# Optimization experiments

Measured on AMD Instinct MI355X. Metric: run time of the kernel, lower is better.

The kernel has to match this reference:

```python
import jax, jax.numpy as jnp
import numpy as np

B, T, C = 32, 128, 64
E, H = 8, 4            # feat_dim, num_heads
D = E // H             # head_dim = 2
HID = 32               # hidden_dim


def setup_inputs() -> dict:
    key = jax.random.key(0)
    ks = jax.random.split(key, 20)
    s = 0.1
    return {
        "x": jax.random.normal(ks[0], (B, T, C), jnp.float32),
        # input_proj: Linear(C, C)
        "W_in": jax.random.normal(ks[1], (C, C), jnp.float32) * s,
        "b_in": jax.random.normal(ks[2], (C,), jnp.float32) * s,
        # time_step_score: Linear(C, C//4) -> GELU -> Linear(C//4, 1) -> Sigmoid
        "W_ts1": jax.random.normal(ks[3], (C // 4, C), jnp.float32) * s,
        "b_ts1": jax.random.normal(ks[4], (C // 4,), jnp.float32) * s,
        "W_ts2": jax.random.normal(ks[5], (1, C // 4), jnp.float32) * s,
        "b_ts2": jax.random.normal(ks[6], (1,), jnp.float32) * s,
        # per-channel GRU(1 -> E): torch gate order (r, z, n)
        "W_ih": jax.random.normal(ks[7], (C, 3 * E), jnp.float32) * s,      # input size 1
        "W_hh": jax.random.normal(ks[8], (C, 3 * E, E), jnp.float32) * s,
        "b_ih": jax.random.normal(ks[9], (C, 3 * E), jnp.float32) * s,
        "b_hh": jax.random.normal(ks[10], (C, 3 * E), jnp.float32) * s,
        # shared MultiheadAttention(E, 4): packed in_proj + out_proj
        "W_qkv": jax.random.normal(ks[11], (3 * E, E), jnp.float32) * s,
        "b_qkv": jax.random.normal(ks[12], (3 * E,), jnp.float32) * s,
        "W_o": jax.random.normal(ks[13], (E, E), jnp.float32) * s,
        "b_o": jax.random.normal(ks[14], (E,), jnp.float32) * s,
        # out_proj: Linear(C*E, HID)
        "W_out": jax.random.normal(ks[15], (HID, C * E), jnp.float32) * s,
        "b_out": jax.random.normal(ks[16], (HID,), jnp.float32) * s,
    }


def _forward(x, W_in, b_in, W_ts1, b_ts1, W_ts2, b_ts2,
             W_ih, W_hh, b_ih, b_hh, W_qkv, b_qkv, W_o, b_o, W_out, b_out):
    bs, ts, c = x.shape
    # time step importance: per-timestep MLP over the raw features
    h1 = jax.nn.gelu(jnp.einsum('btc,fc->btf', x, W_ts1) + b_ts1, approximate=False)
    ts_imp = jax.nn.sigmoid(jnp.einsum('btf,of->bto', h1, W_ts2) + b_ts2)[..., 0]  # [B,T]

    xp = jnp.einsum('btc,dc->btd', x, W_in) + b_in  # [B,T,C]

    # Batched per-channel GRU scan over time. state h: [B,C,E]
    def step(h, x_t):
        gi = x_t[:, :, None] * W_ih[None] + b_ih          # [B,C,3E]
        gh = jnp.einsum('bce,cge->bcg', h, W_hh) + b_hh   # [B,C,3E]
        ir, iz, inn = gi[..., :E], gi[..., E:2 * E], gi[..., 2 * E:]
        hr, hz, hn = gh[..., :E], gh[..., E:2 * E], gh[..., 2 * E:]
        r = jax.nn.sigmoid(ir + hr)
        z = jax.nn.sigmoid(iz + hz)
        n = jnp.tanh(inn + r * hn)
        h_new = (1.0 - z) * n + z * h
        return h_new, h_new

    h0 = jnp.zeros((bs, c, E), xp.dtype)
    _, hs = jax.lax.scan(step, h0, jnp.transpose(xp, (1, 0, 2)))  # [T,B,C,E]
    hs_bcte = jnp.transpose(hs, (1, 2, 0, 3))                     # [B,C,T,E]

    # Shared MHA applied independently per channel (batched over B*C)
    qkv = jnp.einsum('bcte,fe->bctf', hs_bcte, W_qkv) + b_qkv     # [B,C,T,3E]
    q, k, v = qkv[..., :E], qkv[..., E:2 * E], qkv[..., 2 * E:]
    def heads(t):
        return t.reshape(bs, c, ts, H, D)
    q, k, v = heads(q), heads(k), heads(v)
    scores = jnp.einsum('bcthd,bcshd->bchts', q, k) / np.sqrt(D)
    attn = jax.nn.softmax(scores, axis=-1)
    o = jnp.einsum('bchts,bcshd->bcthd', attn, v).reshape(bs, c, ts, E)
    attn_out = jnp.einsum('bcte,fe->bctf', o, W_o) + b_o          # [B,C,T,E]
    attention = jnp.transpose(attn_out, (0, 2, 1, 3))             # [B,T,C,E]

    out_flat = jnp.transpose(hs, (1, 0, 2, 3)).reshape(bs, ts, c * E)  # [B,T,C*E]
    out = jnp.einsum('btf,hf->bth', out_flat, W_out) + b_out           # [B,T,HID]

    feat_imp = jax.nn.sigmoid(attention.sum(axis=(1, 3)))   # [B,C]
    tsf_imp = jax.nn.sigmoid(attention.sum(axis=-1))        # [B,T,C]
    return out[:, -1, :], feat_imp, ts_imp, tsf_imp


def reference(x, W_in, b_in, W_ts1, b_ts1, W_ts2, b_ts2,
              W_ih, W_hh, b_ih, b_hh, W_qkv, b_qkv, W_o, b_o, W_out, b_out):
    return _forward(x, W_in, b_in, W_ts1, b_ts1, W_ts2, b_ts2,
                    W_ih, W_hh, b_ih, b_hh, W_qkv, b_qkv, W_o, b_o, W_out, b_out)
```

## Files before the change

kernel.cpp:

```cpp
#include <hip/hip_runtime.h>
#include <hip/hip_bf16.h>
#include <math.h>

#define B_ 32
#define T_ 128
#define C_ 64
#define E_ 8
#define HID_ 32

#define LOG2E 1.44269504088896341f

__device__ __forceinline__ float fast_rcp(float x) { return __builtin_amdgcn_rcpf(x); }
__device__ __forceinline__ float fast_exp2(float x) { return exp2f(x); }
__device__ __forceinline__ float fast_sigmoid(float x) {
    return fast_rcp(1.0f + fast_exp2(-LOG2E * x));
}
__device__ __forceinline__ float fast_tanh(float x) {
    float xc = __builtin_amdgcn_fmed3f(x, -15.0f, 15.0f);
    float t = fast_exp2(2.0f * LOG2E * xc);
    return (t - 1.0f) * fast_rcp(t + 1.0f);
}

__global__ __launch_bounds__(64) void k_pre(
    const float* __restrict__ x, const float* __restrict__ W_in, const float* __restrict__ b_in,
    float* __restrict__ xp)
{
    const int bt = blockIdx.x;
    const int tid = threadIdx.x;
    __shared__ __align__(16) float4 xs4[16];
    if (tid < 16) xs4[tid] = ((const float4*)(x + bt * C_))[tid];
    __syncthreads();
    float a = b_in[tid];
    const float4* w4 = (const float4*)(W_in + tid * C_);
#pragma unroll
    for (int k4 = 0; k4 < 16; ++k4) {
        float4 xv = xs4[k4];
        float4 wv = w4[k4];
        a = fmaf(xv.x, wv.x, a); a = fmaf(xv.y, wv.y, a);
        a = fmaf(xv.z, wv.z, a); a = fmaf(xv.w, wv.w, a);
    }
    xp[bt * C_ + tid] = a;
}

__global__ __launch_bounds__(64) void k_gru(
    const float* __restrict__ xp, const float* __restrict__ W_ih, const float* __restrict__ W_hh,
    const float* __restrict__ b_ih, const float* __restrict__ b_hh,
    float* __restrict__ hs, float* __restrict__ fh)
{
    const int tid = threadIdx.x;
    const int ci = tid >> 2;
    const int q  = tid & 3;
    const int chain = blockIdx.x * 16 + ci;
    const int c = chain & 63;

    __shared__ float xc[16][T_ + 1];

    const int c_base = (blockIdx.x & 3) * 16;
    const int bb = blockIdx.x >> 2;
    for (int idx = tid; idx < 16 * T_; idx += 64) {
        int cci = idx & 15;
        int t = idx >> 4;
        xc[cci][t] = xp[(bb * T_ + t) * C_ + c_base + cci];
    }
    __syncthreads();

    float wr[2][8], wz[2][8], wn[2][8];
    float wir[2], wiz[2], win_[2], cr[2], cz[2], bin_[2], bhn[2];
#pragma unroll
    for (int u = 0; u < 2; ++u) {
        const int e = 2 * q + u;
#pragma unroll
        for (int m = 0; m < 4; ++m) {
#pragma unroll
            for (int p = 0; p < 2; ++p) {
                const int j = 2 * (q ^ m) + p;
                wr[u][2 * m + p] = W_hh[(c * 24 + 0  + e) * 8 + j];
                wz[u][2 * m + p] = W_hh[(c * 24 + 8  + e) * 8 + j];
                wn[u][2 * m + p] = W_hh[(c * 24 + 16 + e) * 8 + j];
            }
        }
        wir[u] = W_ih[c * 24 + e];
        wiz[u] = W_ih[c * 24 + 8 + e];
        win_[u] = W_ih[c * 24 + 16 + e];
        cr[u] = b_ih[c * 24 + e] + b_hh[c * 24 + e];
        cz[u] = b_ih[c * 24 + 8 + e] + b_hh[c * 24 + 8 + e];
        bin_[u] = b_ih[c * 24 + 16 + e];
        bhn[u]  = b_hh[c * 24 + 16 + e];
    }

    float ha = 0.0f, hb = 0.0f;
    float* hop = hs + (size_t)chain * T_ * E_ + 2 * q;
    float xv = xc[ci][0];
    for (int t = 0; t < T_; ++t) {
        float xvn = xc[ci][t + 1];
        float pa1 = __shfl_xor(ha, 1), pb1 = __shfl_xor(hb, 1);
        float pa2 = __shfl_xor(ha, 2), pb2 = __shfl_xor(hb, 2);
        float pa3 = __shfl_xor(pa1, 2), pb3 = __shfl_xor(pb1, 2);
        const float pa[4] = {ha, pa1, pa2, pa3};
        const float pb[4] = {hb, pb1, pb2, pb3};
        float hnew[2];
#pragma unroll
        for (int u = 0; u < 2; ++u) {
            float g0 = fmaf(pb[0], wr[u][1], pa[0] * wr[u][0]);
            float g1 = fmaf(pb[1], wr[u][3], pa[1] * wr[u][2]);
            float g2 = fmaf(pb[2], wr[u][5], pa[2] * wr[u][4]);
            float g3 = fmaf(pb[3], wr[u][7], pa[3] * wr[u][6]);
            float gr = fmaf(xv, wir[u], cr[u]) + ((g0 + g1) + (g2 + g3));
            float z0 = fmaf(pb[0], wz[u][1], pa[0] * wz[u][0]);
            float z1 = fmaf(pb[1], wz[u][3], pa[1] * wz[u][2]);
            float z2 = fmaf(pb[2], wz[u][5], pa[2] * wz[u][4]);
            float z3 = fmaf(pb[3], wz[u][7], pa[3] * wz[u][6]);
            float gz = fmaf(xv, wiz[u], cz[u]) + ((z0 + z1) + (z2 + z3));
            float n0 = fmaf(pb[0], wn[u][1], pa[0] * wn[u][0]);
            float n1 = fmaf(pb[1], wn[u][3], pa[1] * wn[u][2]);
            float n2 = fmaf(pb[2], wn[u][5], pa[2] * wn[u][4]);
            float n3 = fmaf(pb[3], wn[u][7], pa[3] * wn[u][6]);
            float hn = bhn[u] + ((n0 + n1) + (n2 + n3));
            float gn = fmaf(xv, win_[u], bin_[u]);
            float r = fast_sigmoid(gr);
            float z = fast_sigmoid(gz);
            float nn = fast_tanh(fmaf(r, hn, gn));
            float hu = (u == 0) ? ha : hb;
            hnew[u] = fmaf(z, hu - nn, nn);
        }
        ha = hnew[0]; hb = hnew[1];
        *(float2*)(hop + (size_t)t * E_) = make_float2(ha, hb);
        xv = xvn;
    }
    fh[chain * E_ + 2 * q] = ha;
    fh[chain * E_ + 2 * q + 1] = hb;
}

__global__ __launch_bounds__(256) void k_attn(
    const float* __restrict__ hs, const float* __restrict__ W_qkv, const float* __restrict__ b_qkv,
    const float* __restrict__ W_o, const float* __restrict__ b_o,
    float* __restrict__ feat_imp, float* __restrict__ tsf_imp)
{
    const int bc = blockIdx.x;
    const int b = bc >> 6, c = bc & 63;
    const int tid = threadIdx.x;
    const int t2 = tid & 63;
    const int sq = tid >> 6;

    __shared__ __align__(16) float ks[T_][E_];
    __shared__ __align__(16) float us[T_][4];
    __shared__ float qsT[E_][T_];
    __shared__ float pacc[3][T_][8];
    __shared__ float red[T_];

    const float qscale = 0.70710678118654752f * LOG2E;

    {
        const int row = (tid < 128) ? tid : (tid - 128);
        const float4* hp = (const float4*)(hs + (size_t)bc * T_ * E_ + row * E_);
        float4 h0 = hp[0], h1 = hp[1];
        float hr[E_] = {h0.x, h0.y, h0.z, h0.w, h1.x, h1.y, h1.z, h1.w};
        if (tid < 128) {
            float kv[E_];
#pragma unroll
            for (int f = 0; f < E_; ++f) {
                float a = b_qkv[E_ + f];
#pragma unroll
                for (int j = 0; j < E_; ++j) a = fmaf(hr[j], W_qkv[(E_ + f) * E_ + j], a);
                kv[f] = a;
            }
            ((float4*)&ks[row][0])[0] = make_float4(kv[0], kv[1], kv[2], kv[3]);
            ((float4*)&ks[row][0])[1] = make_float4(kv[4], kv[5], kv[6], kv[7]);
#pragma unroll
            for (int f = 0; f < E_; ++f) {
                float a = b_qkv[f];
#pragma unroll
                for (int j = 0; j < E_; ++j) a = fmaf(hr[j], W_qkv[f * E_ + j], a);
                qsT[f][row] = a * qscale;
            }
        } else {
            float ws[E_];
#pragma unroll
            for (int d = 0; d < E_; ++d) {
                float wv = 0.0f;
#pragma unroll
                for (int fp = 0; fp < E_; ++fp) wv += W_o[fp * E_ + d];
                ws[d] = wv;
            }
            float vv[E_];
#pragma unroll
            for (int f = 0; f < E_; ++f) {
                float a = b_qkv[2 * E_ + f];
#pragma unroll
                for (int j = 0; j < E_; ++j) a = fmaf(hr[j], W_qkv[(2 * E_ + f) * E_ + j], a);
                vv[f] = a;
            }
            float4 uu;
            uu.x = fmaf(vv[1], ws[1], vv[0] * ws[0]);
            uu.y = fmaf(vv[3], ws[3], vv[2] * ws[2]);
            uu.z = fmaf(vv[5], ws[5], vv[4] * ws[4]);
            uu.w = fmaf(vv[7], ws[7], vv[6] * ws[6]);
            *((float4*)&us[row][0]) = uu;
        }
    }
    __syncthreads();

    float q0[E_], q1[E_];
#pragma unroll
    for (int f = 0; f < E_; ++f) { q0[f] = qsT[f][t2]; q1[f] = qsT[f][t2 + 64]; }

    float l0[4] = {0.f,0.f,0.f,0.f}, S0[4] = {0.f,0.f,0.f,0.f};
    float l1[4] = {0.f,0.f,0.f,0.f}, S1[4] = {0.f,0.f,0.f,0.f};
    const float* kb = &ks[sq * 32][0];
    const float* ub = &us[sq * 32][0];
#pragma unroll 8
    for (int i = 0; i < 32; ++i) {
        float4 k0 = *(const float4*)(kb + i * 8);
        float4 k1 = *(const float4*)(kb + i * 8 + 4);
        float4 uu = *(const float4*)(ub + i * 4);
        float p00 = fast_exp2(fmaf(q0[1], k0.y, q0[0] * k0.x));
        float p01 = fast_exp2(fmaf(q0[3], k0.w, q0[2] * k0.z));
        float p02 = fast_exp2(fmaf(q0[5], k1.y, q0[4] * k1.x));
        float p03 = fast_exp2(fmaf(q0[7], k1.w, q0[6] * k1.z));
        float p10 = fast_exp2(fmaf(q1[1], k0.y, q1[0] * k0.x));
        float p11 = fast_exp2(fmaf(q1[3], k0.w, q1[2] * k0.z));
        float p12 = fast_exp2(fmaf(q1[5], k1.y, q1[4] * k1.x));
        float p13 = fast_exp2(fmaf(q1[7], k1.w, q1[6] * k1.z));
        l0[0] += p00; l0[1] += p01; l0[2] += p02; l0[3] += p03;
        l1[0] += p10; l1[1] += p11; l1[2] += p12; l1[3] += p13;
        S0[0] = fmaf(p00, uu.x, S0[0]); S0[1] = fmaf(p01, uu.y, S0[1]);
        S0[2] = fmaf(p02, uu.z, S0[2]); S0[3] = fmaf(p03, uu.w, S0[3]);
        S1[0] = fmaf(p10, uu.x, S1[0]); S1[1] = fmaf(p11, uu.y, S1[1]);
        S1[2] = fmaf(p12, uu.z, S1[2]); S1[3] = fmaf(p13, uu.w, S1[3]);
    }

    if (sq > 0) {
        float* pr = &pacc[sq - 1][t2][0];
#pragma unroll
        for (int i = 0; i < 4; ++i) { pr[i] = l0[i]; pr[4 + i] = S0[i]; }
        pr = &pacc[sq - 1][t2 + 64][0];
#pragma unroll
        for (int i = 0; i < 4; ++i) { pr[i] = l1[i]; pr[4 + i] = S1[i]; }
    }
    __syncthreads();

    if (sq == 0) {
        float bsum = 0.0f;
#pragma unroll
        for (int fp = 0; fp < E_; ++fp) bsum += b_o[fp];
#pragma unroll
        for (int qq = 0; qq < 3; ++qq) {
#pragma unroll
            for (int i = 0; i < 4; ++i) {
                l0[i] += pacc[qq][t2][i];       S0[i] += pacc[qq][t2][4 + i];
                l1[i] += pacc[qq][t2 + 64][i];  S1[i] += pacc[qq][t2 + 64][4 + i];
            }
        }
        float Sa = bsum, Sb = bsum;
#pragma unroll
        for (int hh = 0; hh < 4; ++hh) {
            Sa = fmaf(S0[hh], fast_rcp(l0[hh]), Sa);
            Sb = fmaf(S1[hh], fast_rcp(l1[hh]), Sb);
        }
        tsf_imp[(size_t)b * T_ * C_ + (size_t)t2 * C_ + c] = fast_sigmoid(Sa);
        tsf_imp[(size_t)b * T_ * C_ + (size_t)(t2 + 64) * C_ + c] = fast_sigmoid(Sb);
        red[t2] = Sa;
        red[t2 + 64] = Sb;
    }
    __syncthreads();
    for (int off = 64; off > 0; off >>= 1) {
        if (tid < off) red[tid] += red[tid + off];
        __syncthreads();
    }
    if (tid == 0) feat_imp[bc] = fast_sigmoid(red[0]);
}

__global__ __launch_bounds__(64) void k_ts(
    const float* __restrict__ x,
    const float* __restrict__ W_ts1, const float* __restrict__ b_ts1,
    const float* __restrict__ W_ts2, const float* __restrict__ b_ts2,
    float* __restrict__ ts_imp)
{
    const int bt = blockIdx.x;
    const int tid = threadIdx.x;
    __shared__ float xs[C_];
    __shared__ float h1[16];
    xs[tid] = x[bt * C_ + tid];
    __syncthreads();
    if (tid < 16) {
        float a = b_ts1[tid];
#pragma unroll
        for (int k = 0; k < C_; ++k) a = fmaf(xs[k], W_ts1[tid * C_ + k], a);
        h1[tid] = 0.5f * a * (1.0f + erff(a * 0.70710678118654752f));
    }
    __syncthreads();
    if (tid == 0) {
        float s = b_ts2[0];
#pragma unroll
        for (int k = 0; k < 16; ++k) s = fmaf(h1[k], W_ts2[k], s);
        ts_imp[bt] = fast_sigmoid(s);
    }
}

__global__ __launch_bounds__(64) void k_out(
    const float* __restrict__ fh, const float* __restrict__ W_out, const float* __restrict__ b_out,
    float* __restrict__ out0)
{
    const int b = blockIdx.x;
    const int tid = threadIdx.x;
    __shared__ float hf[C_ * E_];
    const float4* src = (const float4*)(fh + (b * C_ + tid) * E_);
    float4* dst = (float4*)(hf + tid * E_);
    dst[0] = src[0];
    dst[1] = src[1];
    __syncthreads();
    if (tid < HID_) {
        float a = b_out[tid];
        const float* wo = W_out + tid * (C_ * E_);
        for (int k = 0; k < C_ * E_; ++k) a = fmaf(hf[k], wo[k], a);
        out0[b * HID_ + tid] = a;
    }
}

extern "C" void kernel_launch(void* const* d_in, const int* in_sizes, int n_in,
                              void* d_out, int out_size, void* d_ws, size_t ws_size,
                              hipStream_t stream) {
    (void)in_sizes; (void)n_in; (void)out_size; (void)ws_size;

    float* out0 = (float*)d_out;
    float* feat = out0 + B_ * HID_;
    float* tsim = feat + B_ * C_;
    float* tsf  = tsim + B_ * T_;

    const float* x     = (const float*)d_in[0];
    const float* W_in  = (const float*)d_in[1];
    const float* b_in  = (const float*)d_in[2];
    const float* W_ts1 = (const float*)d_in[3];
    const float* b_ts1 = (const float*)d_in[4];
    const float* W_ts2 = (const float*)d_in[5];
    const float* b_ts2 = (const float*)d_in[6];
    const float* W_ih  = (const float*)d_in[7];
    const float* W_hh  = (const float*)d_in[8];
    const float* b_ih  = (const float*)d_in[9];
    const float* b_hh  = (const float*)d_in[10];
    const float* W_qkv = (const float*)d_in[11];
    const float* b_qkv = (const float*)d_in[12];
    const float* W_o   = (const float*)d_in[13];
    const float* b_o   = (const float*)d_in[14];
    const float* W_out = (const float*)d_in[15];
    const float* b_out = (const float*)d_in[16];

    float* fhb = (float*)d_ws;
    float* xpb = fhb + B_ * C_ * E_;
    float* hsb = xpb + (size_t)B_ * T_ * C_;

    hipLaunchKernelGGL(k_pre, dim3(B_ * T_), dim3(64), 0, stream, x, W_in, b_in, xpb);
    hipLaunchKernelGGL(k_gru, dim3(B_ * C_ / 16), dim3(64), 0, stream,
                       xpb, W_ih, W_hh, b_ih, b_hh, hsb, fhb);
    hipLaunchKernelGGL(k_attn, dim3(B_ * C_), dim3(256), 0, stream,
                       hsb, W_qkv, b_qkv, W_o, b_o, feat, tsf);
    hipLaunchKernelGGL(k_ts, dim3(B_ * T_), dim3(64), 0, stream,
                       x, W_ts1, b_ts1, W_ts2, b_ts2, tsim);
    hipLaunchKernelGGL(k_out, dim3(B_), dim3(64), 0, stream,
                       fhb, W_out, b_out, out0);
}
```

Measured before the change: 111.1 us.

## Fuse side kernels into pre and attention launches, use DPP rotations in GRU

Folds the time-step importance MLP into the input projection kernel and the final output projection into an extra block of the attention kernel, cutting five launches to three. The feat_imp reduction now uses wavefront shuffles instead of a shared-memory tree with repeated barriers. In the GRU scan, the cross-lane exchanges switch from xor shuffles to quad DPP rotations, with the weight index permutation changed to match. The single extra block doing the output GEMV could become a tail straggler, and the DPP quad controls must match the rotation-based indexing.

```diff
diff --git a/kernel.cpp b/kernel.cpp
--- a/kernel.cpp
+++ b/kernel.cpp
@@ -21,25 +21,52 @@
     return (t - 1.0f) * fast_rcp(t + 1.0f);
 }
 
-__global__ __launch_bounds__(64) void k_pre(
+template <int CTRL>
+__device__ __forceinline__ float qperm(float v) {
+    return __int_as_float(__builtin_amdgcn_update_dpp(
+        __float_as_int(v), __float_as_int(v), CTRL, 0xF, 0xF, false));
+}
+#define ROT1 0x39
+#define ROT2 0x4E
+#define ROT3 0x93
+
+__global__ __launch_bounds__(64) void k_pre_ts(
     const float* __restrict__ x, const float* __restrict__ W_in, const float* __restrict__ b_in,
-    float* __restrict__ xp)
+    const float* __restrict__ W_ts1, const float* __restrict__ b_ts1,
+    const float* __restrict__ W_ts2, const float* __restrict__ b_ts2,
+    float* __restrict__ xp, float* __restrict__ ts_imp)
 {
     const int bt = blockIdx.x;
     const int tid = threadIdx.x;
-    __shared__ __align__(16) float4 xs4[16];
-    if (tid < 16) xs4[tid] = ((const float4*)(x + bt * C_))[tid];
-    __syncthreads();
+    __shared__ __align__(16) float xs[C_];
+    __shared__ float h1[16];
+    if (tid < 16) ((float4*)xs)[tid] = ((const float4*)(x + bt * C_))[tid];
+    __syncthreads();
+
     float a = b_in[tid];
     const float4* w4 = (const float4*)(W_in + tid * C_);
 #pragma unroll
     for (int k4 = 0; k4 < 16; ++k4) {
-        float4 xv = xs4[k4];
+        float4 xv = ((const float4*)xs)[k4];
         float4 wv = w4[k4];
         a = fmaf(xv.x, wv.x, a); a = fmaf(xv.y, wv.y, a);
         a = fmaf(xv.z, wv.z, a); a = fmaf(xv.w, wv.w, a);
     }
     xp[bt * C_ + tid] = a;
+
+    if (tid < 16) {
+        float s = b_ts1[tid];
+#pragma unroll
+        for (int k = 0; k < C_; ++k) s = fmaf(xs[k], W_ts1[tid * C_ + k], s);
+        h1[tid] = 0.5f * s * (1.0f + erff(s * 0.70710678118654752f));
+    }
+    __syncthreads();
+    if (tid == 0) {
+        float s = b_ts2[0];
+#pragma unroll
+        for (int k = 0; k < 16; ++k) s = fmaf(h1[k], W_ts2[k], s);
+        ts_imp[bt] = fast_sigmoid(s);
+    }
 }
 
 __global__ __launch_bounds__(64) void k_gru(
@@ -73,7 +100,7 @@
         for (int m = 0; m < 4; ++m) {
 #pragma unroll
             for (int p = 0; p < 2; ++p) {
-                const int j = 2 * (q ^ m) + p;
+                const int j = 2 * ((q + m) & 3) + p;
                 wr[u][2 * m + p] = W_hh[(c * 24 + 0  + e) * 8 + j];
                 wz[u][2 * m + p] = W_hh[(c * 24 + 8  + e) * 8 + j];
                 wn[u][2 * m + p] = W_hh[(c * 24 + 16 + e) * 8 + j];
@@ -93,9 +120,9 @@
     float xv = xc[ci][0];
     for (int t = 0; t < T_; ++t) {
         float xvn = xc[ci][t + 1];
-        float pa1 = __shfl_xor(ha, 1), pb1 = __shfl_xor(hb, 1);
-        float pa2 = __shfl_xor(ha, 2), pb2 = __shfl_xor(hb, 2);
-        float pa3 = __shfl_xor(pa1, 2), pb3 = __shfl_xor(pb1, 2);
+        float pa1 = qperm<ROT1>(ha), pb1 = qperm<ROT1>(hb);
+        float pa2 = qperm<ROT2>(ha), pb2 = qperm<ROT2>(hb);
+        float pa3 = qperm<ROT3>(ha), pb3 = qperm<ROT3>(hb);
         const float pa[4] = {ha, pa1, pa2, pa3};
         const float pb[4] = {hb, pb1, pb2, pb3};
         float hnew[2];
@@ -131,14 +158,34 @@
     fh[chain * E_ + 2 * q + 1] = hb;
 }
 
-__global__ __launch_bounds__(256) void k_attn(
+__global__ __launch_bounds__(256) void k_attn_out(
     const float* __restrict__ hs, const float* __restrict__ W_qkv, const float* __restrict__ b_qkv,
     const float* __restrict__ W_o, const float* __restrict__ b_o,
-    float* __restrict__ feat_imp, float* __restrict__ tsf_imp)
+    const float* __restrict__ fh, const float* __restrict__ W_out, const float* __restrict__ b_out,
+    float* __restrict__ out0, float* __restrict__ feat_imp, float* __restrict__ tsf_imp)
 {
+    const int tid = threadIdx.x;
+
+    if (blockIdx.x == B_ * C_) {
+#pragma unroll
+        for (int pi = tid; pi < B_ * HID_; pi += 256) {
+            int bb = pi >> 5, o = pi & 31;
+            const float4* hv = (const float4*)(fh + bb * C_ * E_);
+            const float4* wv = (const float4*)(W_out + o * C_ * E_);
+            float a = b_out[o];
+#pragma unroll 16
+            for (int k4 = 0; k4 < 128; ++k4) {
+                float4 h4 = hv[k4], w4 = wv[k4];
+                a = fmaf(h4.x, w4.x, a); a = fmaf(h4.y, w4.y, a);
+                a = fmaf(h4.z, w4.z, a); a = fmaf(h4.w, w4.w, a);
+            }
+            out0[pi] = a;
+        }
+        return;
+    }
+
     const int bc = blockIdx.x;
     const int b = bc >> 6, c = bc & 63;
-    const int tid = threadIdx.x;
     const int t2 = tid & 63;
     const int sq = tid >> 6;
 
@@ -146,7 +193,6 @@
     __shared__ __align__(16) float us[T_][4];
     __shared__ float qsT[E_][T_];
     __shared__ float pacc[3][T_][8];
-    __shared__ float red[T_];
 
     const float qscale = 0.70710678118654752f * LOG2E;
 
@@ -259,61 +305,10 @@
         }
         tsf_imp[(size_t)b * T_ * C_ + (size_t)t2 * C_ + c] = fast_sigmoid(Sa);
         tsf_imp[(size_t)b * T_ * C_ + (size_t)(t2 + 64) * C_ + c] = fast_sigmoid(Sb);
-        red[t2] = Sa;
-        red[t2 + 64] = Sb;
-    }
-    __syncthreads();
-    for (int off = 64; off > 0; off >>= 1) {
-        if (tid < off) red[tid] += red[tid + off];
-        __syncthreads();
-    }
-    if (tid == 0) feat_imp[bc] = fast_sigmoid(red[0]);
-}
-
-__global__ __launch_bounds__(64) void k_ts(
-    const float* __restrict__ x,
-    const float* __restrict__ W_ts1, const float* __restrict__ b_ts1,
-    const float* __restrict__ W_ts2, const float* __restrict__ b_ts2,
-    float* __restrict__ ts_imp)
-{
-    const int bt = blockIdx.x;
-    const int tid = threadIdx.x;
-    __shared__ float xs[C_];
-    __shared__ float h1[16];
-    xs[tid] = x[bt * C_ + tid];
-    __syncthreads();
-    if (tid < 16) {
-        float a = b_ts1[tid];
-#pragma unroll
-        for (int k = 0; k < C_; ++k) a = fmaf(xs[k], W_ts1[tid * C_ + k], a);
-        h1[tid] = 0.5f * a * (1.0f + erff(a * 0.70710678118654752f));
-    }
-    __syncthreads();
-    if (tid == 0) {
-        float s = b_ts2[0];
-#pragma unroll
-        for (int k = 0; k < 16; ++k) s = fmaf(h1[k], W_ts2[k], s);
-        ts_imp[bt] = fast_sigmoid(s);
-    }
-}
-
-__global__ __launch_bounds__(64) void k_out(
-    const float* __restrict__ fh, const float* __restrict__ W_out, const float* __restrict__ b_out,
-    float* __restrict__ out0)
-{
-    const int b = blockIdx.x;
-    const int tid = threadIdx.x;
-    __shared__ float hf[C_ * E_];
-    const float4* src = (const float4*)(fh + (b * C_ + tid) * E_);
-    float4* dst = (float4*)(hf + tid * E_);
-    dst[0] = src[0];
-    dst[1] = src[1];
-    __syncthreads();
-    if (tid < HID_) {
-        float a = b_out[tid];
-        const float* wo = W_out + tid * (C_ * E_);
-        for (int k = 0; k < C_ * E_; ++k) a = fmaf(hf[k], wo[k], a);
-        out0[b * HID_ + tid] = a;
+        float fsum = Sa + Sb;
+#pragma unroll
+        for (int off = 1; off <= 32; off <<= 1) fsum += __shfl_xor(fsum, off);
+        if (t2 == 0) feat_imp[bc] = fast_sigmoid(fsum);
     }
 }
 
@@ -349,13 +344,11 @@
     float* xpb = fhb + B_ * C_ * E_;
     float* hsb = xpb + (size_t)B_ * T_ * C_;
 
-    hipLaunchKernelGGL(k_pre, dim3(B_ * T_), dim3(64), 0, stream, x, W_in, b_in, xpb);
+    hipLaunchKernelGGL(k_pre_ts, dim3(B_ * T_), dim3(64), 0, stream,
+                       x, W_in, b_in, W_ts1, b_ts1, W_ts2, b_ts2, xpb, tsim);
     hipLaunchKernelGGL(k_gru, dim3(B_ * C_ / 16), dim3(64), 0, stream,
                        xpb, W_ih, W_hh, b_ih, b_hh, hsb, fhb);
-    hipLaunchKernelGGL(k_attn, dim3(B_ * C_), dim3(256), 0, stream,
-                       hsb, W_qkv, b_qkv, W_o, b_o, feat, tsf);
-    hipLaunchKernelGGL(k_ts, dim3(B_ * T_), dim3(64), 0, stream,
-                       x, W_ts1, b_ts1, W_ts2, b_ts2, tsim);
-    hipLaunchKernelGGL(k_out, dim3(B_), dim3(64), 0, stream,
-                       fhb, W_out, b_out, out0);
-}
+    hipLaunchKernelGGL(k_attn_out, dim3(B_ * C_ + 1), dim3(256), 0, stream,
+                       hsb, W_qkv, b_qkv, W_o, b_o,
+                       fhb, W_out, b_out, out0, feat, tsf);
+}
```

New measurement: 160.8 us. +44.7%, slower.

## Fuse timestep MLP into input projection and give GRU one lane per hidden unit

Applied to the files above, without the earlier changes.

The timestep-importance MLP is folded into the input projection kernel so x is loaded once and one launch disappears. The GRU kernel now assigns one lane per hidden element (8 lanes per chain, 8 chains per block) instead of 4 lanes each handling two elements. This halves the per-step serial work and doubles the number of blocks. Hidden-state exchange uses DPP quad-permute and half-mirror moves instead of ds_bpermute shuffles. k_out is moved ahead of k_attn in the launch order.

```diff
diff --git a/kernel.cpp b/kernel.cpp
--- a/kernel.cpp
+++ b/kernel.cpp
@@ -21,25 +21,53 @@
     return (t - 1.0f) * fast_rcp(t + 1.0f);
 }
 
-__global__ __launch_bounds__(64) void k_pre(
+template <int CTRL>
+__device__ __forceinline__ float dppf(float v) {
+    return __int_as_float(__builtin_amdgcn_update_dpp(
+        __float_as_int(v), __float_as_int(v), CTRL, 0xF, 0xF, false));
+}
+#define QP_XOR1 0xB1
+#define QP_XOR2 0x4E
+#define QP_XOR3 0x1B
+#define HALF_MIRROR 0x141
+
+__global__ __launch_bounds__(64) void k_pre_ts(
     const float* __restrict__ x, const float* __restrict__ W_in, const float* __restrict__ b_in,
-    float* __restrict__ xp)
+    const float* __restrict__ W_ts1, const float* __restrict__ b_ts1,
+    const float* __restrict__ W_ts2, const float* __restrict__ b_ts2,
+    float* __restrict__ xp, float* __restrict__ ts_imp)
 {
     const int bt = blockIdx.x;
     const int tid = threadIdx.x;
-    __shared__ __align__(16) float4 xs4[16];
-    if (tid < 16) xs4[tid] = ((const float4*)(x + bt * C_))[tid];
-    __syncthreads();
+    __shared__ __align__(16) float xs[C_];
+    __shared__ float h1[16];
+    if (tid < 16) ((float4*)xs)[tid] = ((const float4*)(x + bt * C_))[tid];
+    __syncthreads();
+
     float a = b_in[tid];
     const float4* w4 = (const float4*)(W_in + tid * C_);
 #pragma unroll
     for (int k4 = 0; k4 < 16; ++k4) {
-        float4 xv = xs4[k4];
+        float4 xv = ((const float4*)xs)[k4];
         float4 wv = w4[k4];
         a = fmaf(xv.x, wv.x, a); a = fmaf(xv.y, wv.y, a);
         a = fmaf(xv.z, wv.z, a); a = fmaf(xv.w, wv.w, a);
     }
     xp[bt * C_ + tid] = a;
+
+    if (tid < 16) {
+        float s = b_ts1[tid];
+#pragma unroll
+        for (int k = 0; k < C_; ++k) s = fmaf(xs[k], W_ts1[tid * C_ + k], s);
+        h1[tid] = 0.5f * s * (1.0f + erff(s * 0.70710678118654752f));
+    }
+    __syncthreads();
+    if (tid == 0) {
+        float s = b_ts2[0];
+#pragma unroll
+        for (int k = 0; k < 16; ++k) s = fmaf(h1[k], W_ts2[k], s);
+        ts_imp[bt] = fast_sigmoid(s);
+    }
 }
 
 __global__ __launch_bounds__(64) void k_gru(
@@ -48,87 +76,73 @@
     float* __restrict__ hs, float* __restrict__ fh)
 {
     const int tid = threadIdx.x;
-    const int ci = tid >> 2;
-    const int q  = tid & 3;
-    const int chain = blockIdx.x * 16 + ci;
+    const int ci = tid >> 3;
+    const int e = tid & 7;
+    const int chain = blockIdx.x * 8 + ci;
     const int c = chain & 63;
 
-    __shared__ float xc[16][T_ + 1];
-
-    const int c_base = (blockIdx.x & 3) * 16;
-    const int bb = blockIdx.x >> 2;
-    for (int idx = tid; idx < 16 * T_; idx += 64) {
-        int cci = idx & 15;
-        int t = idx >> 4;
+    __shared__ float xc[8][T_ + 1];
+
+    const int c_base = (blockIdx.x & 7) * 8;
+    const int bb = blockIdx.x >> 3;
+    for (int idx = tid; idx < 8 * T_; idx += 64) {
+        int cci = idx & 7, t = idx >> 3;
         xc[cci][t] = xp[(bb * T_ + t) * C_ + c_base + cci];
     }
     __syncthreads();
 
-    float wr[2][8], wz[2][8], wn[2][8];
-    float wir[2], wiz[2], win_[2], cr[2], cz[2], bin_[2], bhn[2];
-#pragma unroll
-    for (int u = 0; u < 2; ++u) {
-        const int e = 2 * q + u;
-#pragma unroll
-        for (int m = 0; m < 4; ++m) {
-#pragma unroll
-            for (int p = 0; p < 2; ++p) {
-                const int j = 2 * (q ^ m) + p;
-                wr[u][2 * m + p] = W_hh[(c * 24 + 0  + e) * 8 + j];
-                wz[u][2 * m + p] = W_hh[(c * 24 + 8  + e) * 8 + j];
-                wn[u][2 * m + p] = W_hh[(c * 24 + 16 + e) * 8 + j];
-            }
-        }
-        wir[u] = W_ih[c * 24 + e];
-        wiz[u] = W_ih[c * 24 + 8 + e];
-        win_[u] = W_ih[c * 24 + 16 + e];
-        cr[u] = b_ih[c * 24 + e] + b_hh[c * 24 + e];
-        cz[u] = b_ih[c * 24 + 8 + e] + b_hh[c * 24 + 8 + e];
-        bin_[u] = b_ih[c * 24 + 16 + e];
-        bhn[u]  = b_hh[c * 24 + 16 + e];
-    }
-
-    float ha = 0.0f, hb = 0.0f;
-    float* hop = hs + (size_t)chain * T_ * E_ + 2 * q;
+    float wr[8], wz[8], wn[8];
+#pragma unroll
+    for (int m = 0; m < 8; ++m) {
+        const int j = e ^ m;
+        wr[m] = W_hh[(c * 24 + 0  + e) * 8 + j];
+        wz[m] = W_hh[(c * 24 + 8  + e) * 8 + j];
+        wn[m] = W_hh[(c * 24 + 16 + e) * 8 + j];
+    }
+    const float wir = W_ih[c * 24 + e], wiz = W_ih[c * 24 + 8 + e], win = W_ih[c * 24 + 16 + e];
+    const float cr = b_ih[c * 24 + e] + b_hh[c * 24 + e];
+    const float cz = b_ih[c * 24 + 8 + e] + b_hh[c * 24 + 8 + e];
+    const float bin_ = b_ih[c * 24 + 16 + e];
+    const float bhn  = b_hh[c * 24 + 16 + e];
+
+    float h = 0.0f;
+    float* ho = hs + (size_t)chain * T_ * E_ + e;
     float xv = xc[ci][0];
     for (int t = 0; t < T_; ++t) {
         float xvn = xc[ci][t + 1];
-        float pa1 = __shfl_xor(ha, 1), pb1 = __shfl_xor(hb, 1);
-        float pa2 = __shfl_xor(ha, 2), pb2 = __shfl_xor(hb, 2);
-        float pa3 = __shfl_xor(pa1, 2), pb3 = __shfl_xor(pb1, 2);
-        const float pa[4] = {ha, pa1, pa2, pa3};
-        const float pb[4] = {hb, pb1, pb2, pb3};
-        float hnew[2];
-#pragma unroll
-        for (int u = 0; u < 2; ++u) {
-            float g0 = fmaf(pb[0], wr[u][1], pa[0] * wr[u][0]);
-            float g1 = fmaf(pb[1], wr[u][3], pa[1] * wr[u][2]);
-            float g2 = fmaf(pb[2], wr[u][5], pa[2] * wr[u][4]);
-            float g3 = fmaf(pb[3], wr[u][7], pa[3] * wr[u][6]);
-            float gr = fmaf(xv, wir[u], cr[u]) + ((g0 + g1) + (g2 + g3));
-            float z0 = fmaf(pb[0], wz[u][1], pa[0] * wz[u][0]);
-            float z1 = fmaf(pb[1], wz[u][3], pa[1] * wz[u][2]);
-            float z2 = fmaf(pb[2], wz[u][5], pa[2] * wz[u][4]);
-            float z3 = fmaf(pb[3], wz[u][7], pa[3] * wz[u][6]);
-            float gz = fmaf(xv, wiz[u], cz[u]) + ((z0 + z1) + (z2 + z3));
-            float n0 = fmaf(pb[0], wn[u][1], pa[0] * wn[u][0]);
-            float n1 = fmaf(pb[1], wn[u][3], pa[1] * wn[u][2]);
-            float n2 = fmaf(pb[2], wn[u][5], pa[2] * wn[u][4]);
-            float n3 = fmaf(pb[3], wn[u][7], pa[3] * wn[u][6]);
-            float hn = bhn[u] + ((n0 + n1) + (n2 + n3));
-            float gn = fmaf(xv, win_[u], bin_[u]);
-            float r = fast_sigmoid(gr);
-            float z = fast_sigmoid(gz);
-            float nn = fast_tanh(fmaf(r, hn, gn));
-            float hu = (u == 0) ? ha : hb;
-            hnew[u] = fmaf(z, hu - nn, nn);
-        }
-        ha = hnew[0]; hb = hnew[1];
-        *(float2*)(hop + (size_t)t * E_) = make_float2(ha, hb);
+        float p1 = dppf<QP_XOR1>(h);
+        float p2 = dppf<QP_XOR2>(h);
+        float p3 = dppf<QP_XOR3>(h);
+        float p7 = dppf<HALF_MIRROR>(h);
+        float p6 = dppf<HALF_MIRROR>(p1);
+        float p5 = dppf<HALF_MIRROR>(p2);
+        float p4 = dppf<HALF_MIRROR>(p3);
+        const float pa[8] = {h, p1, p2, p3, p4, p5, p6, p7};
+
+        float g0 = fmaf(pa[1], wr[1], pa[0] * wr[0]);
+        float g1 = fmaf(pa[3], wr[3], pa[2] * wr[2]);
+        float g2 = fmaf(pa[5], wr[5], pa[4] * wr[4]);
+        float g3 = fmaf(pa[7], wr[7], pa[6] * wr[6]);
+        float gr = fmaf(xv, wir, cr) + ((g0 + g1) + (g2 + g3));
+        float z0 = fmaf(pa[1], wz[1], pa[0] * wz[0]);
+        float z1 = fmaf(pa[3], wz[3], pa[2] * wz[2]);
+        float z2 = fmaf(pa[5], wz[5], pa[4] * wz[4]);
+        float z3 = fmaf(pa[7], wz[7], pa[6] * wz[6]);
+        float gz = fmaf(xv, wiz, cz) + ((z0 + z1) + (z2 + z3));
+        float n0 = fmaf(pa[1], wn[1], pa[0] * wn[0]);
+        float n1 = fmaf(pa[3], wn[3], pa[2] * wn[2]);
+        float n2 = fmaf(pa[5], wn[5], pa[4] * wn[4]);
+        float n3 = fmaf(pa[7], wn[7], pa[6] * wn[6]);
+        float hn = bhn + ((n0 + n1) + (n2 + n3));
+        float gn = fmaf(xv, win, bin_);
+        float r = fast_sigmoid(gr);
+        float z = fast_sigmoid(gz);
+        float nn = fast_tanh(fmaf(r, hn, gn));
+        h = fmaf(z, h - nn, nn);
+        ho[t * E_] = h;
         xv = xvn;
     }
-    fh[chain * E_ + 2 * q] = ha;
-    fh[chain * E_ + 2 * q + 1] = hb;
+    fh[chain * E_ + e] = h;
 }
 
 __global__ __launch_bounds__(256) void k_attn(
@@ -270,33 +284,6 @@
     if (tid == 0) feat_imp[bc] = fast_sigmoid(red[0]);
 }
 
-__global__ __launch_bounds__(64) void k_ts(
-    const float* __restrict__ x,
-    const float* __restrict__ W_ts1, const float* __restrict__ b_ts1,
-    const float* __restrict__ W_ts2, const float* __restrict__ b_ts2,
-    float* __restrict__ ts_imp)
-{
-    const int bt = blockIdx.x;
-    const int tid = threadIdx.x;
-    __shared__ float xs[C_];
-    __shared__ float h1[16];
-    xs[tid] = x[bt * C_ + tid];
-    __syncthreads();
-    if (tid < 16) {
-        float a = b_ts1[tid];
-#pragma unroll
-        for (int k = 0; k < C_; ++k) a = fmaf(xs[k], W_ts1[tid * C_ + k], a);
-        h1[tid] = 0.5f * a * (1.0f + erff(a * 0.70710678118654752f));
-    }
-    __syncthreads();
-    if (tid == 0) {
-        float s = b_ts2[0];
-#pragma unroll
-        for (int k = 0; k < 16; ++k) s = fmaf(h1[k], W_ts2[k], s);
-        ts_imp[bt] = fast_sigmoid(s);
-    }
-}
-
 __global__ __launch_bounds__(64) void k_out(
     const float* __restrict__ fh, const float* __restrict__ W_out, const float* __restrict__ b_out,
     float* __restrict__ out0)
@@ -349,13 +336,12 @@
     float* xpb = fhb + B_ * C_ * E_;
     float* hsb = xpb + (size_t)B_ * T_ * C_;
 
-    hipLaunchKernelGGL(k_pre, dim3(B_ * T_), dim3(64), 0, stream, x, W_in, b_in, xpb);
-    hipLaunchKernelGGL(k_gru, dim3(B_ * C_ / 16), dim3(64), 0, stream,
+    hipLaunchKernelGGL(k_pre_ts, dim3(B_ * T_), dim3(64), 0, stream,
+                       x, W_in, b_in, W_ts1, b_ts1, W_ts2, b_ts2, xpb, tsim);
+    hipLaunchKernelGGL(k_gru, dim3(B_ * C_ / 8), dim3(64), 0, stream,
                        xpb, W_ih, W_hh, b_ih, b_hh, hsb, fhb);
+    hipLaunchKernelGGL(k_out, dim3(B_), dim3(64), 0, stream,
+                       fhb, W_out, b_out, out0);
     hipLaunchKernelGGL(k_attn, dim3(B_ * C_), dim3(256), 0, stream,
                        hsb, W_qkv, b_qkv, W_o, b_o, feat, tsf);
-    hipLaunchKernelGGL(k_ts, dim3(B_ * T_), dim3(64), 0, stream,
-                       x, W_ts1, b_ts1, W_ts2, b_ts2, tsim);
-    hipLaunchKernelGGL(k_out, dim3(B_), dim3(64), 0, stream,
-                       fhb, W_out, b_out, out0);
-}
+}
```

After: 93.24 us. 16.1% less time.
